# Optimization experiments

Hardware: AMD Instinct MI355X
Metric: run time of the kernel (lower is better)

## Reference

```python
import jax, jax.numpy as jnp
import numpy as np

B, T, H, P = 16, 2048, 256, 256
DT_MIN, DT_MAX = 1e-3, 1e-1


def _dplr_hippo(n):
    # HiPPO-LegS -> normal (DPLR) approximation, as in standard S5 init
    p = np.sqrt(1.0 + 2.0 * np.arange(n))
    A = -(np.tril(p[:, None] * p[None, :]) - np.diag(np.arange(n)))
    pm = np.sqrt(np.arange(n) + 0.5)
    S = A + pm[:, None] * pm[None, :]
    lam_re = np.mean(np.diagonal(S)) * np.ones(n)
    lam_im, V = np.linalg.eigh(S * -1j)  # S is normal; -1j*S is Hermitian
    return lam_re.astype(np.float32), lam_im.astype(np.float32), V


def setup_inputs() -> dict:
    key = jax.random.key(0)
    k_in, k_mask = jax.random.split(key, 2)
    lam_re, lam_im, V = _dplr_hippo(P)
    rng = np.random.default_rng(0)
    # b: lecun_normal real init, rotated by V^-1 (init_v_inv_b), stored as (P,H,2)
    B0 = rng.standard_normal((P, H)) / np.sqrt(H)
    Bt = V.conj().T @ B0
    b = np.stack([Bt.real, Bt.imag], axis=-1).astype(np.float32)
    # c: truncated-standard-normal-style complex init rotated by V (init_cv), (H,P,2)
    C0 = (rng.standard_normal((H, P)) + 1j * rng.standard_normal((H, P))) * np.sqrt(0.5)
    Ct = C0 @ V
    c = np.stack([Ct.real, Ct.imag], axis=-1).astype(np.float32)
    d = rng.standard_normal(H).astype(np.float32)
    log_step = (rng.uniform(size=P) * (np.log(DT_MAX) - np.log(DT_MIN)) + np.log(DT_MIN)).astype(np.float32)
    return {
        "inputs": jax.random.normal(k_in, (B, T, H), jnp.float32),
        "mask": jax.random.randint(k_mask, (B, T), 0, 2, jnp.int32),
        "carry_re": jnp.zeros((B, P), jnp.float32),
        "carry_im": jnp.zeros((B, P), jnp.float32),
        "lambda_real": jnp.asarray(lam_re),
        "lambda_imag": jnp.asarray(lam_im),
        "b": jnp.asarray(b),
        "c": jnp.asarray(c),
        "d": jnp.asarray(d),
        "log_step": jnp.asarray(log_step),
    }


def _binop_reset(q_i, q_j):
    a_i, b_i, c_i = q_i
    a_j, b_j, c_j = q_j
    c_je = c_j[..., None]
    a_out = a_j * a_i * (1.0 - c_je) + a_j * c_je
    b_out = (a_j * b_i + b_j) * (1.0 - c_je) + b_j * c_je
    c_out = c_i * (1.0 - c_j) + c_j
    return (a_out, b_out, c_out)


def reference(inputs, mask, carry_re, carry_im, lambda_real, lambda_imag, b, c, d, log_step):
    lam = (lambda_real + 1j * lambda_imag).astype(jnp.complex64)      # [P]
    b_tilde = (b[..., 0] + 1j * b[..., 1]).astype(jnp.complex64)       # [P,H]
    c_tilde = (c[..., 0] + 1j * c[..., 1]).astype(jnp.complex64)       # [H,P]
    step = jnp.exp(log_step.astype(jnp.float32)).astype(jnp.complex64)  # step_rescale=1
    # ZOH discretization
    lambda_bar = jnp.exp(lam * step)                                    # [P]
    b_bar = ((lambda_bar - 1.0) / lam)[:, None] * b_tilde               # [P,H]

    u = jnp.swapaxes(inputs, 0, 1)                                      # [T,B,H]
    m = jnp.swapaxes(mask, 0, 1).astype(jnp.float32)                    # [T,B]
    carry = (carry_re + 1j * carry_im).astype(jnp.complex64)            # [B,P]

    t, bsz, h = u.shape
    p = lam.shape[0]
    a = jnp.broadcast_to(lambda_bar[None, None, :], (t, bsz, p))
    a = jnp.concatenate([jnp.ones((1, bsz, p), a.dtype), a], axis=0)    # [T+1,B,P]
    bu = jnp.einsum('ph,tbh->tbp', b_bar, u.astype(jnp.complex64))      # [T,B,P]
    bu = jnp.concatenate([carry[None, ...], bu], axis=0)                # [T+1,B,P]
    m = jnp.concatenate([jnp.zeros((1, bsz), m.dtype), m], axis=0)      # [T+1,B]

    _, xs, _ = jax.lax.associative_scan(_binop_reset, (a, bu, m), axis=0)
    xs = xs[1:]                                                         # [T,B,P]

    y = jnp.einsum('hp,tbp->tbh', c_tilde, xs).real + d * u             # [T,B,H]
    x_t = xs[-1]                                                        # [B,P] complex64
    y = jnp.swapaxes(y.astype(jnp.float32), 0, 1)                       # [B,T,H]
    return (x_t, y)
```

## Files before the change

### kernel.cpp

```cpp
#include <hip/hip_runtime.h>
#include <hip/hip_bf16.h>

#define Bn 16
#define Tn 2048
#define Hn 256
#define Pn 256
#define Ln 64
#define NCn (Tn / Ln)
#define BTn (Bn * Tn)
#define NB  (2 * Pn)

#define BM 128
#define BK 32
#define APAD 40

typedef __attribute__((ext_vector_type(8))) short short8;
typedef __attribute__((ext_vector_type(4))) float f32x4;

__device__ __forceinline__ unsigned short f2bf(float f) {
  unsigned u = __float_as_uint(f);
  return (unsigned short)((u + 0x7FFFu + ((u >> 16) & 1u)) >> 16);
}

__device__ __forceinline__ float2 cmul(float2 a, float2 b) {
  return make_float2(fmaf(a.x, b.x, -(a.y * b.y)), fmaf(a.x, b.y, a.y * b.x));
}

__global__ void k_prep(const float* __restrict__ lam_re,
                       const float* __restrict__ lam_im,
                       const float* __restrict__ log_step,
                       const float* __restrict__ b_in,
                       const float* __restrict__ c_in,
                       float2* __restrict__ lam_bar,
                       unsigned short* __restrict__ b_bfT,
                       unsigned short* __restrict__ c_bfT) {
  const int blk = blockIdx.x;
  const int tid = threadIdx.x;

  float s = expf(log_step[tid]);
  float re = lam_re[tid], im = lam_im[tid];
  float er = expf(re * s);
  float sn, cs;
  sincosf(im * s, &sn, &cs);
  float2 lb = make_float2(er * cs, er * sn);
  if (blk == 0) lam_bar[tid] = lb;

  float denom = re * re + im * im;
  float nx = lb.x - 1.0f, ny = lb.y;
  float2 coef = make_float2((nx * re + ny * im) / denom,
                            (ny * re - nx * im) / denom);

  float2 bt = make_float2(b_in[(tid * Hn + blk) * 2 + 0],
                          b_in[(tid * Hn + blk) * 2 + 1]);
  float2 bb = cmul(coef, bt);
  b_bfT[(size_t)(2 * tid + 0) * Hn + blk] = f2bf(bb.x);
  b_bfT[(size_t)(2 * tid + 1) * Hn + blk] = f2bf(bb.y);

  float cr = c_in[(tid * Pn + blk) * 2 + 0];
  float ci = c_in[(tid * Pn + blk) * 2 + 1];
  c_bfT[(size_t)tid * NB + 2 * blk + 0] = f2bf(cr);
  c_bfT[(size_t)tid * NB + 2 * blk + 1] = f2bf(-ci);
}

__launch_bounds__(256)
__global__ void k_bu_mfma(const float* __restrict__ u,
                          const unsigned short* __restrict__ bT,
                          float* __restrict__ bu) {
  __shared__ unsigned short sA[BM * APAD];
  __shared__ unsigned short sB[BM * APAD];
  const int tid = threadIdx.x;
  const int bm = blockIdx.x, bn = blockIdx.y;
  const int lane = tid & 63, wid = tid >> 6;
  const int wr = wid >> 1, wc = wid & 1;
  const int grp = lane >> 4, l15 = lane & 15;

  const f32x4 vzero = {0.f, 0.f, 0.f, 0.f};
  f32x4 acc[4][4];
#pragma unroll
  for (int i = 0; i < 4; i++)
#pragma unroll
    for (int j = 0; j < 4; j++) acc[i][j] = vzero;

  const int sr = tid >> 1, sseg = (tid & 1) * 16;
  const float* uRow = u + (size_t)(bm * BM + sr) * Hn + sseg;
  const unsigned short* bRow = bT + (size_t)(bn * BM + sr) * Hn + sseg;
  unsigned short* sAw = &sA[sr * APAD + sseg];
  unsigned short* sBw = &sB[sr * APAD + sseg];

  for (int k0 = 0; k0 < Hn; k0 += BK) {
    float4 v0 = *reinterpret_cast<const float4*>(uRow + k0);
    float4 v1 = *reinterpret_cast<const float4*>(uRow + k0 + 4);
    float4 v2 = *reinterpret_cast<const float4*>(uRow + k0 + 8);
    float4 v3 = *reinterpret_cast<const float4*>(uRow + k0 + 12);
    short8 q0 = *reinterpret_cast<const short8*>(bRow + k0);
    short8 q1 = *reinterpret_cast<const short8*>(bRow + k0 + 8);
    short8 p0, p1;
    p0[0] = (short)f2bf(v0.x); p0[1] = (short)f2bf(v0.y);
    p0[2] = (short)f2bf(v0.z); p0[3] = (short)f2bf(v0.w);
    p0[4] = (short)f2bf(v1.x); p0[5] = (short)f2bf(v1.y);
    p0[6] = (short)f2bf(v1.z); p0[7] = (short)f2bf(v1.w);
    p1[0] = (short)f2bf(v2.x); p1[1] = (short)f2bf(v2.y);
    p1[2] = (short)f2bf(v2.z); p1[3] = (short)f2bf(v2.w);
    p1[4] = (short)f2bf(v3.x); p1[5] = (short)f2bf(v3.y);
    p1[6] = (short)f2bf(v3.z); p1[7] = (short)f2bf(v3.w);
    *reinterpret_cast<short8*>(sAw) = p0;
    *reinterpret_cast<short8*>(sAw + 8) = p1;
    *reinterpret_cast<short8*>(sBw) = q0;
    *reinterpret_cast<short8*>(sBw + 8) = q1;
    __syncthreads();

    short8 af[4], bfr[4];
#pragma unroll
    for (int i = 0; i < 4; i++)
      af[i] = *reinterpret_cast<const short8*>(
          &sA[(wr * 64 + i * 16 + l15) * APAD + grp * 8]);
#pragma unroll
    for (int j = 0; j < 4; j++)
      bfr[j] = *reinterpret_cast<const short8*>(
          &sB[(wc * 64 + j * 16 + l15) * APAD + grp * 8]);
#pragma unroll
    for (int i = 0; i < 4; i++)
#pragma unroll
      for (int j = 0; j < 4; j++)
        acc[i][j] = __builtin_amdgcn_mfma_f32_16x16x32_bf16(af[i], bfr[j],
                                                            acc[i][j], 0, 0, 0);
    __syncthreads();
  }

  const int r0 = bm * BM + wr * 64 + grp * 4;
  const int c0 = bn * BM + wc * 64 + l15;
#pragma unroll
  for (int i = 0; i < 4; i++)
#pragma unroll
    for (int j = 0; j < 4; j++) {
#pragma unroll
      for (int r = 0; r < 4; r++)
        bu[(size_t)(r0 + i * 16 + r) * NB + (c0 + j * 16)] = acc[i][j][r];
    }
}

__launch_bounds__(256)
__global__ void k_sum(const float2* __restrict__ bu,
                      const int* __restrict__ mask,
                      const float2* __restrict__ lam_bar,
                      float4* __restrict__ sumAB,
                      float* __restrict__ sumC) {
  const int chunk = blockIdx.x, b = blockIdx.y, p = threadIdx.x;
  const float2 lam = lam_bar[p];
  const float2* buB = bu + (size_t)(b * Tn + chunk * Ln) * Pn;
  const int* mB = mask + b * Tn + chunk * Ln;

  float2 A = make_float2(1.f, 0.f), Bv = make_float2(0.f, 0.f);
  float C = 0.f;
  for (int t = 0; t < Ln; t++) {
    int m = mB[t];
    float2 v = buB[t * Pn + p];
    float2 nA = cmul(lam, A);
    float2 nB = cmul(lam, Bv);
    nB.x += v.x; nB.y += v.y;
    A = m ? lam : nA;
    Bv = m ? v : nB;
    C = m ? 1.f : C;
  }
  size_t o = ((size_t)(b * NCn + chunk)) * Pn + p;
  sumAB[o] = make_float4(A.x, A.y, Bv.x, Bv.y);
  sumC[o] = C;
}

__global__ void k_scan(const float* __restrict__ carry_re,
                       const float* __restrict__ carry_im,
                       const float4* __restrict__ sumAB,
                       const float* __restrict__ sumC,
                       float2* __restrict__ xe) {
  int b = blockIdx.x, p = threadIdx.x;
  float2 x = make_float2(carry_re[b * Pn + p], carry_im[b * Pn + p]);
  for (int k = 0; k < NCn; k++) {
    size_t o = ((size_t)(b * NCn + k)) * Pn + p;
    xe[o] = x;
    float4 ab = sumAB[o];
    float C = sumC[o];
    float2 nx = cmul(make_float2(ab.x, ab.y), x);
    nx.x += ab.z; nx.y += ab.w;
    x = (C != 0.f) ? make_float2(ab.z, ab.w) : nx;
  }
}

__launch_bounds__(256)
__global__ void k_apply(const int* __restrict__ mask,
                        const float2* __restrict__ lam_bar,
                        const float2* __restrict__ xe,
                        float2* __restrict__ bu,
                        float* __restrict__ out_xt,
                        int xt_interleaved) {
  int chunk = blockIdx.x, b = blockIdx.y, p = threadIdx.x;
  int t0 = chunk * Ln;
  float2 x = xe[((size_t)(b * NCn + chunk)) * Pn + p];
  float2 lam = lam_bar[p];
  float2* buB = bu + (size_t)(b * Tn + t0) * Pn;
  const int* mB = mask + b * Tn + t0;

  for (int j0 = 0; j0 < Ln; j0 += 8) {
    float2 v[8];
    int m[8];
#pragma unroll
    for (int q = 0; q < 8; q++) {
      v[q] = buB[(j0 + q) * Pn + p];
      m[q] = mB[j0 + q];
    }
#pragma unroll
    for (int q = 0; q < 8; q++) {
      float2 nx = cmul(lam, x);
      nx.x += v[q].x; nx.y += v[q].y;
      x = m[q] ? v[q] : nx;
      buB[(j0 + q) * Pn + p] = x;
    }
  }
  if (chunk == NCn - 1) {
    if (xt_interleaved) {
      out_xt[(b * Pn + p) * 2 + 0] = x.x;
      out_xt[(b * Pn + p) * 2 + 1] = x.y;
    } else {
      out_xt[b * Pn + p] = x.x;
    }
  }
}

__launch_bounds__(256)
__global__ void k_y_mfma(const float* __restrict__ xs,
                         const unsigned short* __restrict__ cT,
                         const float* __restrict__ u,
                         const float* __restrict__ dvec,
                         float* __restrict__ y) {
  __shared__ unsigned short sA[BM * APAD];
  __shared__ unsigned short sB[BM * APAD];
  const int tid = threadIdx.x;
  const int bm = blockIdx.x, bn = blockIdx.y;
  const int lane = tid & 63, wid = tid >> 6;
  const int wr = wid >> 1, wc = wid & 1;
  const int grp = lane >> 4, l15 = lane & 15;

  const f32x4 vzero = {0.f, 0.f, 0.f, 0.f};
  f32x4 acc[4][4];
#pragma unroll
  for (int i = 0; i < 4; i++)
#pragma unroll
    for (int j = 0; j < 4; j++) acc[i][j] = vzero;

  const int sr = tid >> 1, sseg = (tid & 1) * 16;
  const float* aRow = xs + (size_t)(bm * BM + sr) * NB + sseg;
  const unsigned short* bRow = cT + (size_t)(bn * BM + sr) * NB + sseg;
  unsigned short* sAw = &sA[sr * APAD + sseg];
  unsigned short* sBw = &sB[sr * APAD + sseg];

  for (int k0 = 0; k0 < NB; k0 += BK) {
    float4 v0 = *reinterpret_cast<const float4*>(aRow + k0);
    float4 v1 = *reinterpret_cast<const float4*>(aRow + k0 + 4);
    float4 v2 = *reinterpret_cast<const float4*>(aRow + k0 + 8);
    float4 v3 = *reinterpret_cast<const float4*>(aRow + k0 + 12);
    short8 q0 = *reinterpret_cast<const short8*>(bRow + k0);
    short8 q1 = *reinterpret_cast<const short8*>(bRow + k0 + 8);
    short8 p0, p1;
    p0[0] = (short)f2bf(v0.x); p0[1] = (short)f2bf(v0.y);
    p0[2] = (short)f2bf(v0.z); p0[3] = (short)f2bf(v0.w);
    p0[4] = (short)f2bf(v1.x); p0[5] = (short)f2bf(v1.y);
    p0[6] = (short)f2bf(v1.z); p0[7] = (short)f2bf(v1.w);
    p1[0] = (short)f2bf(v2.x); p1[1] = (short)f2bf(v2.y);
    p1[2] = (short)f2bf(v2.z); p1[3] = (short)f2bf(v2.w);
    p1[4] = (short)f2bf(v3.x); p1[5] = (short)f2bf(v3.y);
    p1[6] = (short)f2bf(v3.z); p1[7] = (short)f2bf(v3.w);
    *reinterpret_cast<short8*>(sAw) = p0;
    *reinterpret_cast<short8*>(sAw + 8) = p1;
    *reinterpret_cast<short8*>(sBw) = q0;
    *reinterpret_cast<short8*>(sBw + 8) = q1;
    __syncthreads();

    short8 af[4], bfr[4];
#pragma unroll
    for (int i = 0; i < 4; i++)
      af[i] = *reinterpret_cast<const short8*>(
          &sA[(wr * 64 + i * 16 + l15) * APAD + grp * 8]);
#pragma unroll
    for (int j = 0; j < 4; j++)
      bfr[j] = *reinterpret_cast<const short8*>(
          &sB[(wc * 64 + j * 16 + l15) * APAD + grp * 8]);
#pragma unroll
    for (int i = 0; i < 4; i++)
#pragma unroll
      for (int j = 0; j < 4; j++)
        acc[i][j] = __builtin_amdgcn_mfma_f32_16x16x32_bf16(af[i], bfr[j],
                                                            acc[i][j], 0, 0, 0);
    __syncthreads();
  }

  const int r0 = bm * BM + wr * 64 + grp * 4;
  const int c0 = bn * BM + wc * 64 + l15;
#pragma unroll
  for (int i = 0; i < 4; i++)
#pragma unroll
    for (int j = 0; j < 4; j++) {
      int col = c0 + j * 16;
      float dv = dvec[col];
#pragma unroll
      for (int r = 0; r < 4; r++) {
        int row = r0 + i * 16 + r;
        y[(size_t)row * Hn + col] =
            fmaf(dv, u[(size_t)row * Hn + col], acc[i][j][r]);
      }
    }
}

extern "C" void kernel_launch(void* const* d_in, const int* in_sizes, int n_in,
                              void* d_out, int out_size, void* d_ws, size_t ws_size,
                              hipStream_t stream) {
  const float* inputs   = (const float*)d_in[0];
  const int*   mask     = (const int*)d_in[1];
  const float* carry_re = (const float*)d_in[2];
  const float* carry_im = (const float*)d_in[3];
  const float* lam_re   = (const float*)d_in[4];
  const float* lam_im   = (const float*)d_in[5];
  const float* b_in     = (const float*)d_in[6];
  const float* c_in     = (const float*)d_in[7];
  const float* d_vec    = (const float*)d_in[8];
  const float* log_step = (const float*)d_in[9];

  const int y_elems = Bn * Tn * Hn;
  const int xt_elems = out_size - y_elems;
  const int xt_interleaved = (xt_elems >= Bn * Pn * 2) ? 1 : 0;

  float* out = (float*)d_out;
  float* out_xt = out;
  float* out_y  = out + xt_elems;

  char* ws = (char*)d_ws;
  size_t off = 0;
  auto alloc = [&](size_t bytes) -> void* {
    void* ptr = ws + off;
    off += (bytes + 255) & ~(size_t)255;
    return ptr;
  };
  float* bu              = (float*)alloc((size_t)BTn * NB * sizeof(float));
  unsigned short* b_bfT  = (unsigned short*)alloc((size_t)NB * Hn * sizeof(short));
  unsigned short* c_bfT  = (unsigned short*)alloc((size_t)Hn * NB * sizeof(short));
  float2* lam_bar        = (float2*)alloc(Pn * sizeof(float2));
  float4* sumAB          = (float4*)alloc((size_t)Bn * NCn * Pn * sizeof(float4));
  float*  sumC           = (float*)alloc((size_t)Bn * NCn * Pn * sizeof(float));
  float2* xe             = (float2*)alloc((size_t)Bn * NCn * Pn * sizeof(float2));
  (void)ws_size; (void)in_sizes; (void)n_in;

  k_prep<<<256, 256, 0, stream>>>(lam_re, lam_im, log_step, b_in, c_in,
                                  lam_bar, b_bfT, c_bfT);
  k_bu_mfma<<<dim3(BTn / BM, NB / BM), 256, 0, stream>>>(inputs, b_bfT, bu);
  k_sum<<<dim3(NCn, Bn), 256, 0, stream>>>((const float2*)bu, mask, lam_bar,
                                           sumAB, sumC);
  k_scan<<<Bn, 256, 0, stream>>>(carry_re, carry_im, sumAB, sumC, xe);
  k_apply<<<dim3(NCn, Bn), 256, 0, stream>>>(mask, lam_bar, xe, (float2*)bu,
                                             out_xt, xt_interleaved);
  k_y_mfma<<<dim3(BTn / BM, Hn / BM), 256, 0, stream>>>(bu, c_bfT, inputs,
                                                        d_vec, out_y);
}
```

Measured before the change: 192.8 us.

## Fuse chunk scan apply with output projection GEMM via shared-memory bf16 states

Merges the apply step of the chunked scan with the y = C·x + D·u GEMM into one kernel. Each block scans a chunk of its batch, writes the bf16 states to shared memory, then runs MFMA against the C matrix read straight from global memory. This drops the full fp32 write and reread of the state tensor. Chunk length is halved to keep shared memory small and raise the block count, which doubles the chunk-summary scan length. The B operand is no longer staged in LDS, and the reused C matrix is reloaded from global/L2 by every block.

```diff
diff --git a/kernel.cpp b/kernel.cpp
--- a/kernel.cpp
+++ b/kernel.cpp
@@ -5,7 +5,7 @@
 #define Tn 2048
 #define Hn 256
 #define Pn 256
-#define Ln 64
+#define Ln 32
 #define NCn (Tn / Ln)
 #define BTn (Bn * Tn)
 #define NB  (2 * Pn)
@@ -13,6 +13,7 @@
 #define BM 128
 #define BK 32
 #define APAD 40
+#define YPAD 8
 
 typedef __attribute__((ext_vector_type(8))) short short8;
 typedef __attribute__((ext_vector_type(4))) float f32x4;
@@ -186,127 +187,99 @@
 }
 
 __launch_bounds__(256)
-__global__ void k_apply(const int* __restrict__ mask,
-                        const float2* __restrict__ lam_bar,
-                        const float2* __restrict__ xe,
-                        float2* __restrict__ bu,
-                        float* __restrict__ out_xt,
-                        int xt_interleaved) {
-  int chunk = blockIdx.x, b = blockIdx.y, p = threadIdx.x;
-  int t0 = chunk * Ln;
-  float2 x = xe[((size_t)(b * NCn + chunk)) * Pn + p];
-  float2 lam = lam_bar[p];
-  float2* buB = bu + (size_t)(b * Tn + t0) * Pn;
-  const int* mB = mask + b * Tn + t0;
-
-  for (int j0 = 0; j0 < Ln; j0 += 8) {
-    float2 v[8];
-    int m[8];
-#pragma unroll
-    for (int q = 0; q < 8; q++) {
-      v[q] = buB[(j0 + q) * Pn + p];
-      m[q] = mB[j0 + q];
+__global__ void k_apply_y(const int* __restrict__ mask,
+                          const float2* __restrict__ lam_bar,
+                          const float2* __restrict__ xe,
+                          const float2* __restrict__ bu,
+                          const unsigned short* __restrict__ cT,
+                          const float* __restrict__ u,
+                          const float* __restrict__ dvec,
+                          float* __restrict__ y,
+                          float* __restrict__ out_xt,
+                          int xt_interleaved) {
+  __shared__ unsigned short sXs[Ln * (NB + YPAD)];
+  const int chunk = blockIdx.x, b = blockIdx.y;
+  const int tid = threadIdx.x;
+  const int t0 = chunk * Ln;
+
+  {
+    const int p = tid;
+    float2 x = xe[((size_t)(b * NCn + chunk)) * Pn + p];
+    const float2 lam = lam_bar[p];
+    const float2* buB = bu + (size_t)(b * Tn + t0) * Pn;
+    const int* mB = mask + b * Tn + t0;
+
+    for (int j0 = 0; j0 < Ln; j0 += 8) {
+      float2 v[8];
+      int m[8];
+#pragma unroll
+      for (int q = 0; q < 8; q++) {
+        v[q] = buB[(j0 + q) * Pn + p];
+        m[q] = mB[j0 + q];
+      }
+#pragma unroll
+      for (int q = 0; q < 8; q++) {
+        float2 nx = cmul(lam, x);
+        nx.x += v[q].x; nx.y += v[q].y;
+        x = m[q] ? v[q] : nx;
+        unsigned pk = (unsigned)f2bf(x.x) | ((unsigned)f2bf(x.y) << 16);
+        *reinterpret_cast<unsigned*>(&sXs[(j0 + q) * (NB + YPAD) + 2 * p]) = pk;
+      }
     }
-#pragma unroll
-    for (int q = 0; q < 8; q++) {
-      float2 nx = cmul(lam, x);
-      nx.x += v[q].x; nx.y += v[q].y;
-      x = m[q] ? v[q] : nx;
-      buB[(j0 + q) * Pn + p] = x;
+    if (chunk == NCn - 1) {
+      if (xt_interleaved) {
+        out_xt[(b * Pn + p) * 2 + 0] = x.x;
+        out_xt[(b * Pn + p) * 2 + 1] = x.y;
+      } else {
+        out_xt[b * Pn + p] = x.x;
+      }
     }
   }
-  if (chunk == NCn - 1) {
-    if (xt_interleaved) {
-      out_xt[(b * Pn + p) * 2 + 0] = x.x;
-      out_xt[(b * Pn + p) * 2 + 1] = x.y;
-    } else {
-      out_xt[b * Pn + p] = x.x;
-    }
-  }
-}
-
-__launch_bounds__(256)
-__global__ void k_y_mfma(const float* __restrict__ xs,
-                         const unsigned short* __restrict__ cT,
-                         const float* __restrict__ u,
-                         const float* __restrict__ dvec,
-                         float* __restrict__ y) {
-  __shared__ unsigned short sA[BM * APAD];
-  __shared__ unsigned short sB[BM * APAD];
-  const int tid = threadIdx.x;
-  const int bm = blockIdx.x, bn = blockIdx.y;
-  const int lane = tid & 63, wid = tid >> 6;
-  const int wr = wid >> 1, wc = wid & 1;
+  __syncthreads();
+
+  const int lane = tid & 63, w = tid >> 6;
   const int grp = lane >> 4, l15 = lane & 15;
+  const int n0 = w * 64;
 
   const f32x4 vzero = {0.f, 0.f, 0.f, 0.f};
-  f32x4 acc[4][4];
-#pragma unroll
-  for (int i = 0; i < 4; i++)
+  f32x4 acc[2][4];
+#pragma unroll
+  for (int i = 0; i < 2; i++)
 #pragma unroll
     for (int j = 0; j < 4; j++) acc[i][j] = vzero;
 
-  const int sr = tid >> 1, sseg = (tid & 1) * 16;
-  const float* aRow = xs + (size_t)(bm * BM + sr) * NB + sseg;
-  const unsigned short* bRow = cT + (size_t)(bn * BM + sr) * NB + sseg;
-  unsigned short* sAw = &sA[sr * APAD + sseg];
-  unsigned short* sBw = &sB[sr * APAD + sseg];
-
   for (int k0 = 0; k0 < NB; k0 += BK) {
-    float4 v0 = *reinterpret_cast<const float4*>(aRow + k0);
-    float4 v1 = *reinterpret_cast<const float4*>(aRow + k0 + 4);
-    float4 v2 = *reinterpret_cast<const float4*>(aRow + k0 + 8);
-    float4 v3 = *reinterpret_cast<const float4*>(aRow + k0 + 12);
-    short8 q0 = *reinterpret_cast<const short8*>(bRow + k0);
-    short8 q1 = *reinterpret_cast<const short8*>(bRow + k0 + 8);
-    short8 p0, p1;
-    p0[0] = (short)f2bf(v0.x); p0[1] = (short)f2bf(v0.y);
-    p0[2] = (short)f2bf(v0.z); p0[3] = (short)f2bf(v0.w);
-    p0[4] = (short)f2bf(v1.x); p0[5] = (short)f2bf(v1.y);
-    p0[6] = (short)f2bf(v1.z); p0[7] = (short)f2bf(v1.w);
-    p1[0] = (short)f2bf(v2.x); p1[1] = (short)f2bf(v2.y);
-    p1[2] = (short)f2bf(v2.z); p1[3] = (short)f2bf(v2.w);
-    p1[4] = (short)f2bf(v3.x); p1[5] = (short)f2bf(v3.y);
-    p1[6] = (short)f2bf(v3.z); p1[7] = (short)f2bf(v3.w);
-    *reinterpret_cast<short8*>(sAw) = p0;
-    *reinterpret_cast<short8*>(sAw + 8) = p1;
-    *reinterpret_cast<short8*>(sBw) = q0;
-    *reinterpret_cast<short8*>(sBw + 8) = q1;
-    __syncthreads();
-
-    short8 af[4], bfr[4];
-#pragma unroll
-    for (int i = 0; i < 4; i++)
+    short8 af[2], bfr[4];
+#pragma unroll
+    for (int i = 0; i < 2; i++)
       af[i] = *reinterpret_cast<const short8*>(
-          &sA[(wr * 64 + i * 16 + l15) * APAD + grp * 8]);
+          &sXs[(i * 16 + l15) * (NB + YPAD) + k0 + grp * 8]);
 #pragma unroll
     for (int j = 0; j < 4; j++)
       bfr[j] = *reinterpret_cast<const short8*>(
-          &sB[(wc * 64 + j * 16 + l15) * APAD + grp * 8]);
-#pragma unroll
-    for (int i = 0; i < 4; i++)
+          &cT[(size_t)(n0 + j * 16 + l15) * NB + k0 + grp * 8]);
+#pragma unroll
+    for (int i = 0; i < 2; i++)
 #pragma unroll
       for (int j = 0; j < 4; j++)
         acc[i][j] = __builtin_amdgcn_mfma_f32_16x16x32_bf16(af[i], bfr[j],
                                                             acc[i][j], 0, 0, 0);
-    __syncthreads();
-  }
-
-  const int r0 = bm * BM + wr * 64 + grp * 4;
-  const int c0 = bn * BM + wc * 64 + l15;
-#pragma unroll
-  for (int i = 0; i < 4; i++)
-#pragma unroll
-    for (int j = 0; j < 4; j++) {
-      int col = c0 + j * 16;
-      float dv = dvec[col];
+  }
+
+#pragma unroll
+  for (int j = 0; j < 4; j++) {
+    const int h = n0 + j * 16 + l15;
+    const float dv = dvec[h];
+#pragma unroll
+    for (int i = 0; i < 2; i++) {
+      const int tl0 = i * 16 + grp * 4;
 #pragma unroll
       for (int r = 0; r < 4; r++) {
-        int row = r0 + i * 16 + r;
-        y[(size_t)row * Hn + col] =
-            fmaf(dv, u[(size_t)row * Hn + col], acc[i][j][r]);
+        const size_t row = (size_t)(b * Tn + t0 + tl0 + r);
+        y[row * Hn + h] = fmaf(dv, u[row * Hn + h], acc[i][j][r]);
       }
     }
+  }
 }
 
 extern "C" void kernel_launch(void* const* d_in, const int* in_sizes, int n_in,
@@ -353,8 +326,8 @@
   k_sum<<<dim3(NCn, Bn), 256, 0, stream>>>((const float2*)bu, mask, lam_bar,
                                            sumAB, sumC);
   k_scan<<<Bn, 256, 0, stream>>>(carry_re, carry_im, sumAB, sumC, xe);
-  k_apply<<<dim3(NCn, Bn), 256, 0, stream>>>(mask, lam_bar, xe, (float2*)bu,
-                                             out_xt, xt_interleaved);
-  k_y_mfma<<<dim3(BTn / BM, Hn / BM), 256, 0, stream>>>(bu, c_bfT, inputs,
-                                                        d_vec, out_y);
-}
+  k_apply_y<<<dim3(NCn, Bn), 256, 0, stream>>>(mask, lam_bar, xe,
+                                               (const float2*)bu, c_bfT,
+                                               inputs, d_vec, out_y, out_xt,
+                                               xt_interleaved);
+}
```

Result: slower. 202.1 us (+4.8%).
